# Kernel optimization log

Measured on AMD Instinct MI355X. Metric: run time of the kernel, lower is better.

Reference implementation:

```python
import jax, jax.numpy as jnp
import numpy as np

NUM_HEADS = 16

def setup_inputs() -> dict:
    key = jax.random.key(0)
    k1, k2, k3 = jax.random.split(key, 3)
    B, N, C = 4, 2048, 1024
    x = jax.random.normal(k1, (B, N, C), dtype=jnp.float32)
    # torch Linear weights are [out_features, in_features]
    w_qkv = jax.random.normal(k2, (3 * C, C), dtype=jnp.float32) * (1.0 / np.sqrt(C))
    w_out = jax.random.normal(k3, (C, C), dtype=jnp.float32) * (1.0 / np.sqrt(C))
    b_out = jnp.zeros((C,), dtype=jnp.float32)
    return {"x": x, "w_qkv": w_qkv, "w_out": w_out, "b_out": b_out}

def reference(x, w_qkv, w_out, b_out):
    B, N, C = x.shape
    H = NUM_HEADS
    D = C // H
    scale = 1.0 / np.sqrt(D).astype(np.float32)
    # qkv projection: [B,N,3C] -> [3,B,H,N,D]
    qkv = (x @ w_qkv.T).reshape(B, N, 3, H, D).transpose(2, 0, 3, 1, 4)
    q, k, v = qkv[0], qkv[1], qkv[2]
    # The torch module's block-wise online softmax telescopes to exact softmax.
    scores = jnp.einsum("bhqd,bhkd->bhqk", q, k) * scale
    attn = jax.nn.softmax(scores, axis=-1)
    out = jnp.einsum("bhqk,bhkd->bhqd", attn, v)  # [B,H,N,D]
    out = out.transpose(0, 2, 1, 3).reshape(B, N, C)
    return out @ w_out.T + b_out
```

## Files before the change

kernel.cpp:

```cpp
#include <hip/hip_runtime.h>

typedef __attribute__((ext_vector_type(8))) short vbf8;
typedef __attribute__((ext_vector_type(4))) float vf4;

#define GLOAD16(g, l) __builtin_amdgcn_global_load_lds( \
    (const __attribute__((address_space(1))) void*)(g),  \
    (__attribute__((address_space(3))) void*)(l), 16, 0, 0)

__device__ __forceinline__ unsigned short f2bf(float f) {
  union { float f; unsigned u; } v; v.f = f;
  return (unsigned short)((v.u + 0x7fffu + ((v.u >> 16) & 1u)) >> 16);
}

__device__ __forceinline__ unsigned short cvt_bf16(float f) {
  __bf16 h = (__bf16)f;
  union { __bf16 h; unsigned short u; } v; v.h = h;
  return v.u;
}

__device__ __forceinline__ vf4 mfma16(vbf8 a, vbf8 b, vf4 c) {
  return __builtin_amdgcn_mfma_f32_16x16x32_bf16(a, b, c, 0, 0, 0);
}

__device__ __forceinline__ int swz(int row, int col) {
  return row * 64 + (col ^ ((row & 7) << 3));
}

__global__ __launch_bounds__(256)
void k_cvt_all(const float* __restrict__ x, unsigned short* __restrict__ xo,
               const float* __restrict__ w1, unsigned short* __restrict__ w1o,
               const float* __restrict__ w2, unsigned short* __restrict__ w2o) {
  for (int i = blockIdx.x * blockDim.x + threadIdx.x; i < 3145728; i += gridDim.x * blockDim.x) {
    const float* in; unsigned short* out; int j;
    if (i < 2097152)      { in = x;  out = xo;  j = i; }
    else if (i < 2883584) { in = w1; out = w1o; j = i - 2097152; }
    else                  { in = w2; out = w2o; j = i - 2883584; }
    float4 v = ((const float4*)in)[j];
    ushort4 o;
    o.x = f2bf(v.x); o.y = f2bf(v.y); o.z = f2bf(v.z); o.w = f2bf(v.w);
    ((ushort4*)out)[j] = o;
  }
}

__global__ __launch_bounds__(256, 2)
void k_gemm_qkv(const unsigned short* __restrict__ A,
                const unsigned short* __restrict__ B,
                unsigned short* __restrict__ qb,
                unsigned short* __restrict__ kb,
                unsigned short* __restrict__ vtb) {
  __shared__ unsigned short As[128 * 64];
  __shared__ unsigned short Bs[128 * 64];
  const int tid = threadIdx.x;
  const int lane = tid & 63;
  const int wid = tid >> 6;
  const int wm = wid >> 1, wn = wid & 1;
  const int flat = blockIdx.y * 24 + blockIdx.x;
  const int sw = (flat & 7) * 192 + (flat >> 3);
  const int m0 = (sw / 24) * 128;
  const int n0 = (sw % 24) * 128;
  const int l15 = lane & 15, kg = lane >> 4;
  const int srow = wid * 32 + (lane >> 3);
  const int scol = (lane & 7) * 8;

  vf4 acc[4][4] = {};

  for (int kt = 0; kt < 16; ++kt) {
    __syncthreads();
    const unsigned short* gA = A + (size_t)(m0 + srow) * 1024 + kt * 64 + scol;
    const unsigned short* gB = B + (size_t)(n0 + srow) * 1024 + kt * 64 + scol;
    const unsigned ab = (unsigned)(wid * 32 * 64);
#pragma unroll
    for (int i = 0; i < 4; ++i) {
      GLOAD16(gA + (size_t)i * 8 * 1024, &As[ab + i * 8 * 64]);
      GLOAD16(gB + (size_t)i * 8 * 1024, &Bs[ab + i * 8 * 64]);
    }
    __syncthreads();
#pragma unroll
    for (int kk = 0; kk < 2; ++kk) {
      vbf8 af[4], bfr[4];
#pragma unroll
      for (int mi = 0; mi < 4; ++mi)
        af[mi] = *(const vbf8*)&As[(wm * 64 + mi * 16 + l15) * 64 + kk * 32 + kg * 8];
#pragma unroll
      for (int ni = 0; ni < 4; ++ni)
        bfr[ni] = *(const vbf8*)&Bs[(wn * 64 + ni * 16 + l15) * 64 + kk * 32 + kg * 8];
#pragma unroll
      for (int mi = 0; mi < 4; ++mi)
#pragma unroll
        for (int ni = 0; ni < 4; ++ni)
          acc[mi][ni] = mfma16(af[mi], bfr[ni], acc[mi][ni]);
    }
  }

#pragma unroll
  for (int ni = 0; ni < 4; ++ni) {
    const int c = n0 + wn * 64 + ni * 16 + l15;
    const int which = c >> 10;
    const int hd = c & 1023;
    const int h = hd >> 6, d = hd & 63;
#pragma unroll
    for (int mi = 0; mi < 4; ++mi) {
      if (which == 2) {
        const int m = m0 + wm * 64 + mi * 16 + kg * 4;
        const int b = m >> 11, nn = m & 2047;
        ushort4 pk;
        pk.x = f2bf(acc[mi][ni][0]);
        pk.y = f2bf(acc[mi][ni][1]);
        pk.z = f2bf(acc[mi][ni][2]);
        pk.w = f2bf(acc[mi][ni][3]);
        *(ushort4*)&vtb[((size_t)(b * 16 + h) * 64 + d) * 2048 + nn] = pk;
      } else {
        unsigned short* dst = (which == 0) ? qb : kb;
        const float sc = (which == 0) ? 0.18033688011112042f : 1.0f;
#pragma unroll
        for (int r = 0; r < 4; ++r) {
          const int m = m0 + wm * 64 + mi * 16 + kg * 4 + r;
          const int b = m >> 11, nn = m & 2047;
          dst[(((size_t)(b * 16 + h)) * 2048 + nn) * 64 + d] = f2bf(acc[mi][ni][r] * sc);
        }
      }
    }
  }
}

__global__ __launch_bounds__(512, 4)
void k_attn(const unsigned short* __restrict__ qb,
            const unsigned short* __restrict__ kb,
            const unsigned short* __restrict__ vt,
            unsigned short* __restrict__ ob) {
  __shared__ unsigned short Ks[2][64 * 64];
  __shared__ unsigned short Vs[64 * 64];
  __shared__ unsigned short Ps[8][32][64];
  const int tid = threadIdx.x, lane = tid & 63, w = tid >> 6;
  const int l15 = lane & 15, kg = lane >> 4;
  const int flat = blockIdx.x;
  const int sw = (flat & 7) * 64 + (flat >> 3);
  const int qt = sw & 7, bh = sw >> 3;

  const unsigned short* Q = qb + ((size_t)bh * 2048 + qt * 256 + w * 32) * 64;
  vbf8 qf[2][2];
#pragma unroll
  for (int qj = 0; qj < 2; ++qj)
#pragma unroll
    for (int kk = 0; kk < 2; ++kk)
      qf[qj][kk] = *(const vbf8*)(Q + (qj * 16 + l15) * 64 + kk * 32 + kg * 8);

  vbf8 onesv;
#pragma unroll
  for (int i = 0; i < 8; ++i) onesv[i] = (short)0x3F80;

  vf4 oacc[2][4] = {};
  vf4 lacc[2] = {};

  const int srow = lane >> 3;
  const int scol = (((lane & 7) ^ srow) * 8);
  const int pswz = (l15 & 7) << 3;
  const unsigned short* gKbase = kb + ((size_t)bh * 2048 + w * 8 + srow) * 64 + scol;
  const unsigned short* gVbase = vt + ((size_t)bh * 64 + w * 8 + srow) * 2048 + scol;

#define STAGE_K(t, b) do { \
    GLOAD16(gKbase + (size_t)(t) * 4096, &Ks[b][(w * 8) * 64]); \
  } while (0)
#define STAGE_V(t) do { \
    GLOAD16(gVbase + (size_t)(t) * 64, &Vs[(w * 8) * 64]); \
  } while (0)

  STAGE_K(0, 0);
  asm volatile("s_waitcnt vmcnt(0)" ::: "memory");
  __builtin_amdgcn_s_barrier();
  __builtin_amdgcn_sched_barrier(0);

  for (int kt = 0; kt < 32; ++kt) {
    const int cur = kt & 1;
    STAGE_V(kt);
    if (kt + 1 < 32) STAGE_K(kt + 1, cur ^ 1);

    vbf8 kfr[2][4];
#pragma unroll
    for (int kk = 0; kk < 2; ++kk)
#pragma unroll
      for (int ni = 0; ni < 4; ++ni)
        kfr[kk][ni] = *(const vbf8*)&Ks[cur][swz(ni * 16 + l15, kk * 32 + kg * 8)];

    vf4 s[2][4] = {};
    __builtin_amdgcn_s_setprio(1);
#pragma unroll
    for (int kk = 0; kk < 2; ++kk)
#pragma unroll
      for (int ni = 0; ni < 4; ++ni) {
        s[0][ni] = mfma16(kfr[kk][ni], qf[0][kk], s[0][ni]);
        s[1][ni] = mfma16(kfr[kk][ni], qf[1][kk], s[1][ni]);
      }
    __builtin_amdgcn_s_setprio(0);

#pragma unroll
    for (int qj = 0; qj < 2; ++qj)
#pragma unroll
      for (int ni = 0; ni < 4; ++ni) {
        ushort4 pk;
        pk.x = cvt_bf16(__builtin_amdgcn_exp2f(s[qj][ni][0]));
        pk.y = cvt_bf16(__builtin_amdgcn_exp2f(s[qj][ni][1]));
        pk.z = cvt_bf16(__builtin_amdgcn_exp2f(s[qj][ni][2]));
        pk.w = cvt_bf16(__builtin_amdgcn_exp2f(s[qj][ni][3]));
        *(ushort4*)&Ps[w][qj * 16 + l15][(ni * 16 + kg * 4) ^ pswz] = pk;
      }

    if (kt + 1 < 32) asm volatile("s_waitcnt vmcnt(1) lgkmcnt(0)" ::: "memory");
    else             asm volatile("s_waitcnt vmcnt(0) lgkmcnt(0)" ::: "memory");
    __builtin_amdgcn_s_barrier();
    __builtin_amdgcn_sched_barrier(0);

    __builtin_amdgcn_s_setprio(1);
#pragma unroll
    for (int kk = 0; kk < 2; ++kk) {
      const vbf8 pf0 = *(const vbf8*)&Ps[w][l15][(kk * 32 + kg * 8) ^ pswz];
      const vbf8 pf1 = *(const vbf8*)&Ps[w][16 + l15][(kk * 32 + kg * 8) ^ pswz];
      lacc[0] = mfma16(pf0, onesv, lacc[0]);
      lacc[1] = mfma16(pf1, onesv, lacc[1]);
#pragma unroll
      for (int ni = 0; ni < 4; ++ni) {
        const vbf8 vf = *(const vbf8*)&Vs[swz(ni * 16 + l15, kk * 32 + kg * 8)];
        oacc[0][ni] = mfma16(pf0, vf, oacc[0][ni]);
        oacc[1][ni] = mfma16(pf1, vf, oacc[1][ni]);
      }
    }
    __builtin_amdgcn_s_setprio(0);

    __syncthreads();
  }
#undef STAGE_K
#undef STAGE_V

  const int b = bh >> 4, h = bh & 15;
#pragma unroll
  for (int qj = 0; qj < 2; ++qj)
#pragma unroll
    for (int r = 0; r < 4; ++r) {
      const float inv = 1.0f / lacc[qj][r];
      const int q = qt * 256 + w * 32 + qj * 16 + kg * 4 + r;
#pragma unroll
      for (int ni = 0; ni < 4; ++ni)
        ob[((size_t)b * 2048 + q) * 1024 + h * 64 + ni * 16 + l15] = cvt_bf16(oacc[qj][ni][r] * inv);
    }
}

__global__ __launch_bounds__(256, 2)
void k_gemm_out(const unsigned short* __restrict__ A,
                const unsigned short* __restrict__ B,
                const float* __restrict__ bias,
                float* __restrict__ out) {
  __shared__ unsigned short As[128 * 64];
  __shared__ unsigned short Bs[128 * 64];
  const int tid = threadIdx.x;
  const int lane = tid & 63;
  const int wid = tid >> 6;
  const int wm = wid >> 1, wn = wid & 1;
  const int flat = blockIdx.y * 8 + blockIdx.x;
  const int sw = (flat & 7) * 64 + (flat >> 3);
  const int m0 = (sw / 8) * 128;
  const int n0 = (sw % 8) * 128;
  const int l15 = lane & 15, kg = lane >> 4;
  const int srow = wid * 32 + (lane >> 3);
  const int scol = (lane & 7) * 8;

  vf4 acc[4][4] = {};

  for (int kt = 0; kt < 16; ++kt) {
    __syncthreads();
    const unsigned short* gA = A + (size_t)(m0 + srow) * 1024 + kt * 64 + scol;
    const unsigned short* gB = B + (size_t)(n0 + srow) * 1024 + kt * 64 + scol;
    const unsigned ab = (unsigned)(wid * 32 * 64);
#pragma unroll
    for (int i = 0; i < 4; ++i) {
      GLOAD16(gA + (size_t)i * 8 * 1024, &As[ab + i * 8 * 64]);
      GLOAD16(gB + (size_t)i * 8 * 1024, &Bs[ab + i * 8 * 64]);
    }
    __syncthreads();
#pragma unroll
    for (int kk = 0; kk < 2; ++kk) {
      vbf8 af[4], bfr[4];
#pragma unroll
      for (int mi = 0; mi < 4; ++mi)
        af[mi] = *(const vbf8*)&As[(wm * 64 + mi * 16 + l15) * 64 + kk * 32 + kg * 8];
#pragma unroll
      for (int ni = 0; ni < 4; ++ni)
        bfr[ni] = *(const vbf8*)&Bs[(wn * 64 + ni * 16 + l15) * 64 + kk * 32 + kg * 8];
#pragma unroll
      for (int mi = 0; mi < 4; ++mi)
#pragma unroll
        for (int ni = 0; ni < 4; ++ni)
          acc[mi][ni] = mfma16(af[mi], bfr[ni], acc[mi][ni]);
    }
  }

#pragma unroll
  for (int ni = 0; ni < 4; ++ni) {
    const int c = n0 + wn * 64 + ni * 16 + l15;
    const float bv = bias[c];
#pragma unroll
    for (int mi = 0; mi < 4; ++mi) {
#pragma unroll
      for (int r = 0; r < 4; ++r) {
        const int m = m0 + wm * 64 + mi * 16 + kg * 4 + r;
        out[(size_t)m * 1024 + c] = acc[mi][ni][r] + bv;
      }
    }
  }
}

extern "C" void kernel_launch(void* const* d_in, const int* in_sizes, int n_in,
                              void* d_out, int out_size, void* d_ws, size_t ws_size,
                              hipStream_t stream) {
  const float* x     = (const float*)d_in[0];
  const float* w_qkv = (const float*)d_in[1];
  const float* w_out = (const float*)d_in[2];
  const float* b_out = (const float*)d_in[3];
  float* out = (float*)d_out;

  char* ws = (char*)d_ws;
  unsigned short* xbf   = (unsigned short*)(ws);
  unsigned short* wqkvb = (unsigned short*)(ws + 16777216);
  unsigned short* woutb = (unsigned short*)(ws + 23068672);
  unsigned short* qbuf  = (unsigned short*)(ws + 25165824);
  unsigned short* kbuf  = (unsigned short*)(ws + 41943040);
  unsigned short* vtbuf = (unsigned short*)(ws + 75497472);
  unsigned short* aob   = xbf;

  k_cvt_all<<<2048, 256, 0, stream>>>(x, xbf, w_qkv, wqkvb, w_out, woutb);

  k_gemm_qkv<<<dim3(24, 64), 256, 0, stream>>>(xbf, wqkvb, qbuf, kbuf, vtbuf);
  k_attn<<<dim3(512), 512, 0, stream>>>(qbuf, kbuf, vtbuf, aob);
  k_gemm_out<<<dim3(8, 64), 256, 0, stream>>>(aob, woutb, b_out, out);
}
```

Baseline: 186.0 us.

## Restructure QKV GEMM to 256x256 tiles with double-buffered swizzled LDS pipeline

```diff
diff --git a/kernel.cpp b/kernel.cpp
--- a/kernel.cpp
+++ b/kernel.cpp
@@ -42,82 +42,109 @@
   }
 }
 
-__global__ __launch_bounds__(256, 2)
+__global__ __launch_bounds__(512, 2)
 void k_gemm_qkv(const unsigned short* __restrict__ A,
                 const unsigned short* __restrict__ B,
                 unsigned short* __restrict__ qb,
                 unsigned short* __restrict__ kb,
                 unsigned short* __restrict__ vtb) {
-  __shared__ unsigned short As[128 * 64];
-  __shared__ unsigned short Bs[128 * 64];
+  __shared__ __attribute__((aligned(16))) unsigned short lds[65536];
   const int tid = threadIdx.x;
   const int lane = tid & 63;
-  const int wid = tid >> 6;
-  const int wm = wid >> 1, wn = wid & 1;
-  const int flat = blockIdx.y * 24 + blockIdx.x;
-  const int sw = (flat & 7) * 192 + (flat >> 3);
-  const int m0 = (sw / 24) * 128;
-  const int n0 = (sw % 24) * 128;
+  const int w = tid >> 6;
+  const int wm = w >> 2, wn = w & 3;
   const int l15 = lane & 15, kg = lane >> 4;
-  const int srow = wid * 32 + (lane >> 3);
-  const int scol = (lane & 7) * 8;
-
-  vf4 acc[4][4] = {};
-
-  for (int kt = 0; kt < 16; ++kt) {
-    __syncthreads();
-    const unsigned short* gA = A + (size_t)(m0 + srow) * 1024 + kt * 64 + scol;
-    const unsigned short* gB = B + (size_t)(n0 + srow) * 1024 + kt * 64 + scol;
-    const unsigned ab = (unsigned)(wid * 32 * 64);
-#pragma unroll
-    for (int i = 0; i < 4; ++i) {
-      GLOAD16(gA + (size_t)i * 8 * 1024, &As[ab + i * 8 * 64]);
-      GLOAD16(gB + (size_t)i * 8 * 1024, &Bs[ab + i * 8 * 64]);
-    }
-    __syncthreads();
+  const int flat = blockIdx.x;
+  const int sw = (flat & 7) * 48 + (flat >> 3);
+  const int m0 = (sw / 12) * 256;
+  const int n0 = (sw % 12) * 256;
+
+  const int srow = lane >> 3;
+  const int scg = (lane & 7) ^ srow;
+  const unsigned short* gA = A + (size_t)(m0 + w * 16 + srow) * 1024 + scg * 8;
+  const unsigned short* gB = B + (size_t)(n0 + w * 16 + srow) * 1024 + scg * 8;
+  const unsigned ldsw = (unsigned)(w * 16 * 64);
+
+#define STG(T, kt, h, b) do { \
+    const unsigned short* g_ = (T) ? gB : gA; \
+    unsigned short* l_ = &lds[(T) * 32768 + ((b) * 2 + (h)) * 8192 + ldsw]; \
+    GLOAD16(g_ + (size_t)((h) * 128) * 1024 + (kt) * 64,     l_); \
+    GLOAD16(g_ + (size_t)((h) * 128 + 8) * 1024 + (kt) * 64, l_ + 8 * 64); \
+  } while (0)
+
+  STG(0, 0, 0, 0); STG(1, 0, 0, 0); STG(0, 0, 1, 0); STG(1, 0, 1, 0);
+  asm volatile("s_waitcnt vmcnt(0)" ::: "memory");
+  __builtin_amdgcn_s_barrier();
+  __builtin_amdgcn_sched_barrier(0);
+
+  vf4 acc[8][4] = {};
+  const int rsw = l15 & 7;
+
+  for (int t = 0; t < 16; ++t) {
+    const int b = t & 1;
+    vbf8 bf[4];
 #pragma unroll
     for (int kk = 0; kk < 2; ++kk) {
-      vbf8 af[4], bfr[4];
-#pragma unroll
-      for (int mi = 0; mi < 4; ++mi)
-        af[mi] = *(const vbf8*)&As[(wm * 64 + mi * 16 + l15) * 64 + kk * 32 + kg * 8];
-#pragma unroll
-      for (int ni = 0; ni < 4; ++ni)
-        bfr[ni] = *(const vbf8*)&Bs[(wn * 64 + ni * 16 + l15) * 64 + kk * 32 + kg * 8];
-#pragma unroll
-      for (int mi = 0; mi < 4; ++mi)
-#pragma unroll
-        for (int ni = 0; ni < 4; ++ni)
-          acc[mi][ni] = mfma16(af[mi], bfr[ni], acc[mi][ni]);
-    }
-  }
-
-#pragma unroll
-  for (int ni = 0; ni < 4; ++ni) {
-    const int c = n0 + wn * 64 + ni * 16 + l15;
+#pragma unroll
+      for (int qm = 0; qm < 2; ++qm) {
+        const int ph = kk * 2 + qm;
+        vbf8 af[4];
+        const unsigned abase = (unsigned)((b * 2 + wm) * 8192);
+#pragma unroll
+        for (int mi = 0; mi < 4; ++mi)
+          af[mi] = *(const vbf8*)&lds[abase + (qm * 64 + mi * 16 + l15) * 64 + ((kk * 4 + kg) ^ rsw) * 8];
+        if (qm == 0) {
+          const unsigned bbase = (unsigned)(32768 + (b * 2 + (wn >> 1)) * 8192);
+#pragma unroll
+          for (int nif = 0; nif < 4; ++nif)
+            bf[nif] = *(const vbf8*)&lds[bbase + ((wn & 1) * 64 + nif * 16 + l15) * 64 + ((kk * 4 + kg) ^ rsw) * 8];
+        }
+        if (t < 15) {
+          if (ph == 0) { STG(0, t + 1, 0, b ^ 1); STG(1, t + 1, 0, b ^ 1); }
+          if (ph == 1) { STG(0, t + 1, 1, b ^ 1); STG(1, t + 1, 1, b ^ 1); }
+        }
+
+        __builtin_amdgcn_s_barrier();
+        asm volatile("s_waitcnt lgkmcnt(0)" ::: "memory");
+        __builtin_amdgcn_sched_barrier(0);
+        __builtin_amdgcn_s_setprio(1);
+#pragma unroll
+        for (int mi = 0; mi < 4; ++mi)
+#pragma unroll
+          for (int nif = 0; nif < 4; ++nif)
+            acc[qm * 4 + mi][nif] = mfma16(af[mi], bf[nif], acc[qm * 4 + mi][nif]);
+        __builtin_amdgcn_s_setprio(0);
+        if (ph == 3 && t < 15)
+          asm volatile("s_waitcnt vmcnt(0)" ::: "memory");
+        __builtin_amdgcn_s_barrier();
+      }
+    }
+  }
+#undef STG
+
+#pragma unroll
+  for (int nif = 0; nif < 4; ++nif) {
+    const int c = n0 + wn * 64 + nif * 16 + l15;
     const int which = c >> 10;
     const int hd = c & 1023;
     const int h = hd >> 6, d = hd & 63;
 #pragma unroll
-    for (int mi = 0; mi < 4; ++mi) {
+    for (int mi = 0; mi < 8; ++mi) {
+      const int m = m0 + wm * 128 + mi * 16 + kg * 4;
+      const int bb = m >> 11, nn = m & 2047;
       if (which == 2) {
-        const int m = m0 + wm * 64 + mi * 16 + kg * 4;
-        const int b = m >> 11, nn = m & 2047;
         ushort4 pk;
-        pk.x = f2bf(acc[mi][ni][0]);
-        pk.y = f2bf(acc[mi][ni][1]);
-        pk.z = f2bf(acc[mi][ni][2]);
-        pk.w = f2bf(acc[mi][ni][3]);
-        *(ushort4*)&vtb[((size_t)(b * 16 + h) * 64 + d) * 2048 + nn] = pk;
+        pk.x = f2bf(acc[mi][nif][0]);
+        pk.y = f2bf(acc[mi][nif][1]);
+        pk.z = f2bf(acc[mi][nif][2]);
+        pk.w = f2bf(acc[mi][nif][3]);
+        *(ushort4*)&vtb[((size_t)(bb * 16 + h) * 64 + d) * 2048 + nn] = pk;
       } else {
         unsigned short* dst = (which == 0) ? qb : kb;
         const float sc = (which == 0) ? 0.18033688011112042f : 1.0f;
 #pragma unroll
-        for (int r = 0; r < 4; ++r) {
-          const int m = m0 + wm * 64 + mi * 16 + kg * 4 + r;
-          const int b = m >> 11, nn = m & 2047;
-          dst[(((size_t)(b * 16 + h)) * 2048 + nn) * 64 + d] = f2bf(acc[mi][ni][r] * sc);
-        }
+        for (int r = 0; r < 4; ++r)
+          dst[((size_t)(bb * 16 + h) * 2048 + nn + r) * 64 + d] = f2bf(acc[mi][nif][r] * sc);
       }
     }
   }
@@ -328,7 +355,7 @@
 
   k_cvt_all<<<2048, 256, 0, stream>>>(x, xbf, w_qkv, wqkvb, w_out, woutb);
 
-  k_gemm_qkv<<<dim3(24, 64), 256, 0, stream>>>(xbf, wqkvb, qbuf, kbuf, vtbuf);
+  k_gemm_qkv<<<dim3(384), 512, 0, stream>>>(xbf, wqkvb, qbuf, kbuf, vtbuf);
   k_attn<<<dim3(512), 512, 0, stream>>>(qbuf, kbuf, vtbuf, aob);
   k_gemm_out<<<dim3(8, 64), 256, 0, stream>>>(aob, woutb, b_out, out);
 }
```

Measured after the change: 192.8 us. 3.7% more time.
